# Kernel optimization log

Measured on AMD Instinct MI355X. Metric: run time of the kernel, lower is better.

The kernel has to match this reference:

```python
import jax, jax.numpy as jnp
import numpy as np
from jax import lax

K_TOP = 4
NF1, NF2 = 6, 14
KS1, KS2 = 7, 5


def conv1d_grouped(x, w, b, groups, pad):
    # x: (B, Cin, L), w: (Cout, Cin//groups, K)
    y = lax.conv_general_dilated(x, w, window_strides=(1,), padding=[(pad, pad)],
                                 dimension_numbers=('NCH', 'OIH', 'NCH'),
                                 feature_group_count=groups)
    return y + b[None, :, None]


def kmax_pool(x, k):
    # order-preserving k-max along last axis
    idx = jnp.sort(lax.top_k(x, k)[1], axis=-1)
    return jnp.take_along_axis(x, idx, axis=-1)


def fold_sum(h, b, nf, rows, L):
    # h: (B, rows*nf, L) with group-major channel layout (rows groups of nf)
    h = h.reshape(b, rows, nf, L).transpose(0, 2, 1, 3)        # (B, nf, rows, L)
    h = h.reshape(b, nf, rows // 2, 2, L).sum(axis=3)          # Fold(2,2): sum adjacent row pairs
    return h.transpose(0, 2, 1, 3).reshape(b, (rows // 2) * nf, L)


def setup_inputs() -> dict:
    key = jax.random.key(0)
    ks = jax.random.split(key, 8)
    V, D, C, B, S = 50257, 256, 1000, 32, 1024
    x = jax.random.randint(ks[0], (B, S), 0, V)
    emb = jax.random.normal(ks[1], (V, D), jnp.float32)
    w1 = jax.random.normal(ks[2], (NF1 * D, 1, KS1), jnp.float32) * 0.1
    b1 = jnp.zeros((NF1 * D,), jnp.float32)
    w2 = jax.random.normal(ks[3], (NF2 * (D // 2), NF1, KS2), jnp.float32) * 0.05
    b2 = jnp.zeros((NF2 * (D // 2),), jnp.float32)
    wf = jax.random.normal(ks[4], (C, NF2 * (D // 4) * K_TOP), jnp.float32) * 0.02
    bf = jnp.zeros((C,), jnp.float32)
    return {"x": x, "emb": emb, "w1": w1, "b1": b1, "w2": w2, "b2": b2, "wf": wf, "bf": bf}


def reference(x, emb, w1, b1, w2, b2, wf, bf):
    D = emb.shape[1]
    B = x.shape[0]
    h = emb[x].transpose(0, 2, 1)                 # (B, D, S)
    h = conv1d_grouped(h, w1, b1, groups=D, pad=KS1 - 1)   # (B, 6D, S+6)
    L1 = h.shape[-1]
    h = fold_sum(h, B, NF1, D, L1)                # (B, 3D, L1)
    # dynamic k-max: layer 1 of 2 -> k = max(k_top, ceil(L/2))
    k1 = max(K_TOP, -(-L1 // 2))
    h = jnp.tanh(kmax_pool(h, k1))
    h = conv1d_grouped(h, w2, b2, groups=D // 2, pad=KS2 - 1)  # (B, 7D, k1+4)
    L2 = h.shape[-1]
    h = fold_sum(h, B, NF2, D // 2, L2)           # (B, 14*(D/4), L2)
    h = jnp.tanh(kmax_pool(h, K_TOP))             # (B, 14*(D/4), k_top)
    # dropout is identity in eval mode
    h = h.reshape(B, -1)
    return h @ wf.T + bf
```

## Files before the change

### kernel.cpp

```cpp
#include <hip/hip_runtime.h>
#include <hip/hip_bf16.h>


typedef __attribute__((ext_vector_type(8))) short short8;
typedef __attribute__((ext_vector_type(4))) float f32x4;

__device__ __forceinline__ float fast_tanh(float x) {
    float e = __expf(2.f * x);
    return 1.f - 2.f / (e + 1.f);
}

__device__ __forceinline__ unsigned fkey(float f) {
    unsigned u = __float_as_uint(f);
    return (u & 0x80000000u) ? ~u : (u | 0x80000000u);
}

__device__ __forceinline__ float fkey_inv(unsigned k) {
    unsigned u = (k & 0x80000000u) ? (k ^ 0x80000000u) : ~k;
    return __uint_as_float(u);
}

__device__ __forceinline__ unsigned short f2bf_rne(float f) {
    unsigned u = __float_as_uint(f);
    return (unsigned short)((u + 0x7fffu + ((u >> 16) & 1u)) >> 16);
}

__global__ __launch_bounds__(256) void gather_kernel(
    const int* __restrict__ x, const float* __restrict__ emb, float* __restrict__ E2)
{
    const int b = blockIdx.x >> 4;
    const int c64 = blockIdx.x & 15;
    const int wv = threadIdx.x >> 6, lane = threadIdx.x & 63;
    float* dst = E2 + ((((size_t)b << 6) + lane) << 12);
#pragma unroll
    for (int t = 0; t < 16; ++t) {
        int l = (c64 << 6) + (wv << 4) + t;
        int tok = x[(b << 10) + l];
        float4 v = *(const float4*)(emb + ((size_t)tok << 8) + (lane << 2));
        *(float4*)(dst + (size_t)l * 4) = v;
    }
}

__global__ __launch_bounds__(896) void stage12_kernel(
    const int* __restrict__ x, const float* __restrict__ emb,
    const float* __restrict__ w1, const float* __restrict__ b1,
    const float* __restrict__ w2, const float* __restrict__ b2,
    const float* __restrict__ E2,
    __hip_bfloat16* __restrict__ H)
{
    __shared__ __align__(16) float X[8512];
    __shared__ __align__(16) float F[12 * 536];
    const int b = blockIdx.x >> 6;
    const int r2 = blockIdx.x & 63;
    const int tid = threadIdx.x;
    float* e = X;

    for (int i = tid; i < 12 * 536; i += 896) F[i] = 0.f;
    if (E2) {
        const float* E2blk = E2 + ((((size_t)b << 6) + r2) << 12);
        for (int idx = tid; idx < 1104; idx += 896) {
            int l = idx - 6;
            float4 v = {0.f, 0.f, 0.f, 0.f};
            if (l >= 0 && l < 1024) v = *(const float4*)(E2blk + (size_t)l * 4);
            e[0 * 1104 + idx] = v.x; e[1 * 1104 + idx] = v.y;
            e[2 * 1104 + idx] = v.z; e[3 * 1104 + idx] = v.w;
        }
    } else {
        for (int idx = tid; idx < 1104; idx += 896) {
            int l = idx - 6;
            float4 v = {0.f, 0.f, 0.f, 0.f};
            if (l >= 0 && l < 1024) {
                int tok = x[(b << 10) + l];
                v = *(const float4*)(emb + ((size_t)tok << 8) + (r2 << 2));
            }
            e[0 * 1104 + idx] = v.x; e[1 * 1104 + idx] = v.y;
            e[2 * 1104 + idx] = v.z; e[3 * 1104 + idx] = v.w;
        }
    }
    __syncthreads();

    const int w = tid >> 6;
    const int lane = tid & 63;

    if (w < 12) {
        const int half = (w >= 6) ? 1 : 0;
        const int f = w - half * 6;
        const float* ep0 = e + (2 * half) * 1104;
        const float* ep1 = ep0 + 1104;
        const int c0 = __builtin_amdgcn_readfirstlane((2 * (2 * r2 + half)) * 6 + f);
        const int c1 = c0 + 6;
        float wA[7], wB[7];
#pragma unroll
        for (int t = 0; t < 7; ++t) { wA[t] = w1[c0 * 7 + t]; wB[t] = w1[c1 * 7 + t]; }
        const float bias = b1[c0] + b1[c1];

        const int pos0 = lane * 17;
        float a0[7], a1[7];
#pragma unroll
        for (int t = 0; t < 7; ++t) { a0[t] = ep0[pos0 + t]; a1[t] = ep1[pos0 + t]; }

        unsigned key[17];
#pragma unroll
        for (int j = 0; j < 17; ++j) {
            float a = bias;
#pragma unroll
            for (int t = 0; t < 7; ++t) a += a0[t] * wA[t] + a1[t] * wB[t];
            key[j] = (pos0 + j < 1030) ? fkey(a) : 0u;
            if (j < 16) {
#pragma unroll
                for (int t = 0; t < 6; ++t) { a0[t] = a0[t + 1]; a1[t] = a1[t + 1]; }
                a0[6] = ep0[pos0 + j + 7];
                a1[6] = ep1[pos0 + j + 7];
            }
        }

        unsigned T = 0u;
        for (int bit = 31; bit >= 0; --bit) {
            unsigned cand = T | (1u << bit);
            int cnt = 0;
#pragma unroll
            for (int j = 0; j < 17; ++j) cnt += (int)__popcll(__ballot(key[j] >= cand));
            if (cnt >= 515) T = cand;
            if (cnt == 515) break;
        }

        const unsigned long long lm = (1ull << lane) - 1ull;
        int gt_tot = 0, gt_run = 0, eq_run = 0;
#pragma unroll
        for (int j = 0; j < 17; ++j) {
            unsigned long long bg = __ballot(key[j] > T);
            unsigned long long be = __ballot(key[j] == T);
            gt_tot += (int)__popcll(bg);
            gt_run += (int)__popcll(bg & lm);
            eq_run += (int)__popcll(be & lm);
        }
        const int q = 515 - gt_tot;
        float* Frow = F + w * 536;
#pragma unroll
        for (int j = 0; j < 17; ++j) {
            bool isgt = key[j] > T;
            bool iseq = key[j] == T;
            int pos = gt_run + (eq_run < q ? eq_run : q);
            if (isgt || (iseq && eq_run < q)) Frow[4 + pos] = fast_tanh(fkey_inv(key[j]));
            gt_run += isgt ? 1 : 0;
            eq_run += iseq ? 1 : 0;
        }
    }
    __syncthreads();

    const int jA = lane & 15;
    const int q3 = lane >> 4;
    float* OUT = X;
    short8 Ah0, Ah1, Al0, Al1;
    {
        float wt[16];
#pragma unroll
        for (int mm = 0; mm < 16; ++mm) {
            float v = 0.f;
            if (mm < 15 && jA < 14) {
                const int irow = 3 * q3 + mm / 5;
                const int t = mm % 5;
                const int h2 = (irow >= 6) ? 1 : 0;
                v = w2[(((2 * r2 + h2) * 14 + jA) * 6 + (irow - 6 * h2)) * 5 + t];
            }
            wt[mm] = v;
        }
#pragma unroll
        for (int m = 0; m < 8; ++m) {
            unsigned short h0 = f2bf_rne(wt[m]);
            float fh0 = __uint_as_float((unsigned)h0 << 16);
            Ah0[m] = (short)h0;
            Al0[m] = (short)f2bf_rne(wt[m] - fh0);
            unsigned short h1 = f2bf_rne(wt[8 + m]);
            float fh1 = __uint_as_float((unsigned)h1 << 16);
            Ah1[m] = (short)h1;
            Al1[m] = (short)f2bf_rne(wt[8 + m] - fh1);
        }
    }
    for (int tile = w; tile < 33; tile += 14) {
        const int p0 = tile << 4;
        const int bidx = (3 * q3) * 536 + p0 + jA;
        float fv[16];
#pragma unroll
        for (int mm = 0; mm < 15; ++mm) fv[mm] = F[bidx + (mm / 5) * 536 + (mm % 5)];
        fv[15] = 0.f;
        short8 Bh0, Bh1, Bl0, Bl1;
#pragma unroll
        for (int m = 0; m < 8; ++m) {
            unsigned short h0 = f2bf_rne(fv[m]);
            float fh0 = __uint_as_float((unsigned)h0 << 16);
            Bh0[m] = (short)h0;
            Bl0[m] = (short)f2bf_rne(fv[m] - fh0);
            unsigned short h1 = f2bf_rne(fv[8 + m]);
            float fh1 = __uint_as_float((unsigned)h1 << 16);
            Bh1[m] = (short)h1;
            Bl1[m] = (short)f2bf_rne(fv[8 + m] - fh1);
        }
        f32x4 d0 = {0.f, 0.f, 0.f, 0.f};
        d0 = __builtin_amdgcn_mfma_f32_16x16x32_bf16(Ah0, Bh0, d0, 0, 0, 0);
        d0 = __builtin_amdgcn_mfma_f32_16x16x32_bf16(Ah1, Bh1, d0, 0, 0, 0);
        d0 = __builtin_amdgcn_mfma_f32_16x16x32_bf16(Ah0, Bl0, d0, 0, 0, 0);
        d0 = __builtin_amdgcn_mfma_f32_16x16x32_bf16(Ah1, Bl1, d0, 0, 0, 0);
        d0 = __builtin_amdgcn_mfma_f32_16x16x32_bf16(Al0, Bh0, d0, 0, 0, 0);
        d0 = __builtin_amdgcn_mfma_f32_16x16x32_bf16(Al1, Bh1, d0, 0, 0, 0);
        float* orow = OUT + (q3 * 4) * 532 + p0 + jA;
#pragma unroll
        for (int r = 0; r < 4; ++r) orow[r * 532] = d0[r];
    }
    __syncthreads();

    {
        const int j = w;
        const int base = lane * 9;
        const int bidx2 = __builtin_amdgcn_readfirstlane((2 * r2) * 14 + j);
        const float bias2 = b2[bidx2] + b2[bidx2 + 14];
        float vv[9];
#pragma unroll
        for (int jj = 0; jj < 9; ++jj)
            vv[jj] = (base + jj < 519) ? OUT[j * 532 + base + jj] : -INFINITY;
        float sv[4]; int si[4];
#pragma unroll
        for (int it = 0; it < 4; ++it) {
            float m = vv[0]; int mi = base;
#pragma unroll
            for (int jj = 1; jj < 9; ++jj) { if (vv[jj] > m) { m = vv[jj]; mi = base + jj; } }
#pragma unroll
            for (int d = 1; d < 64; d <<= 1) {
                float om = __shfl_xor(m, d, 64);
                int omi = __shfl_xor(mi, d, 64);
                if (om > m || (om == m && omi < mi)) { m = om; mi = omi; }
            }
            sv[it] = m; si[it] = mi;
            int lj = mi - base;
#pragma unroll
            for (int jj = 0; jj < 9; ++jj) if (jj == lj) vv[jj] = -INFINITY;
        }
#define CSWAP(a, bq) { if (si[a] > si[bq]) { int ti = si[a]; si[a] = si[bq]; si[bq] = ti; \
                                             float tv = sv[a]; sv[a] = sv[bq]; sv[bq] = tv; } }
        CSWAP(0, 1) CSWAP(2, 3) CSWAP(0, 2) CSWAP(1, 3) CSWAP(1, 2)
#undef CSWAP
        if (lane == 0) {
            __hip_bfloat16* op = H + (size_t)b * 3584 + (r2 * 14 + j) * 4;
#pragma unroll
            for (int k = 0; k < 4; ++k) op[k] = __float2bfloat16(fast_tanh(sv[k] + bias2));
        }
    }
}

__global__ __launch_bounds__(256) void bias_init_kernel(
    const float* __restrict__ bfv, float* __restrict__ out)
{
    int idx = blockIdx.x * 256 + threadIdx.x;
    if (idx < 32000) out[idx] = bfv[idx - (idx / 1000) * 1000];
}

__global__ __launch_bounds__(256) void stage3_kernel(
    const __hip_bfloat16* __restrict__ Hb, const float* __restrict__ wf,
    float* __restrict__ out)
{
    __shared__ __align__(16) float sred[2 * 4 * 256];
    const int nt = blockIdx.x % 63;
    const int kc = blockIdx.x / 63;
    const int w = threadIdx.x >> 6, lane = threadIdx.x & 63;
    const int row = lane & 15, quad = lane >> 4;
    const int c = nt * 16 + row;
    const bool cvalid = (c < 1000);
    const int kofs = kc * 896 + w * 224 + quad * 8;
    const __hip_bfloat16* ap0 = Hb + (size_t)row * 3584 + kofs;
    const __hip_bfloat16* ap1 = ap0 + (size_t)16 * 3584;
    const float* bp = wf + (size_t)(cvalid ? c : 0) * 3584 + kofs;

    f32x4 acc0 = {0.f, 0.f, 0.f, 0.f};
    f32x4 acc1 = {0.f, 0.f, 0.f, 0.f};
#pragma unroll
    for (int it = 0; it < 7; ++it) {
        short8 a0 = *(const short8*)(ap0 + it * 32);
        short8 a1 = *(const short8*)(ap1 + it * 32);
        float4 p0 = *(const float4*)(bp + it * 32);
        float4 p1 = *(const float4*)(bp + it * 32 + 4);
        short8 bfr;
        bfr[0] = (short)f2bf_rne(p0.x); bfr[1] = (short)f2bf_rne(p0.y);
        bfr[2] = (short)f2bf_rne(p0.z); bfr[3] = (short)f2bf_rne(p0.w);
        bfr[4] = (short)f2bf_rne(p1.x); bfr[5] = (short)f2bf_rne(p1.y);
        bfr[6] = (short)f2bf_rne(p1.z); bfr[7] = (short)f2bf_rne(p1.w);
        if (!cvalid) bfr = short8{0, 0, 0, 0, 0, 0, 0, 0};
        acc0 = __builtin_amdgcn_mfma_f32_16x16x32_bf16(a0, bfr, acc0, 0, 0, 0);
        acc1 = __builtin_amdgcn_mfma_f32_16x16x32_bf16(a1, bfr, acc1, 0, 0, 0);
    }
#pragma unroll
    for (int r_ = 0; r_ < 4; ++r_) {
        sred[(0 * 4 + w) * 256 + lane * 4 + r_] = acc0[r_];
        sred[(1 * 4 + w) * 256 + lane * 4 + r_] = acc1[r_];
    }
    __syncthreads();
    if (threadIdx.x < 128) {
        const int mt = threadIdx.x >> 6;
        const int l2 = threadIdx.x & 63;
        const int rr = l2 & 15, qq = l2 >> 4;
        const int cc = nt * 16 + rr;
        if (cc < 1000) {
            const float* sp = sred + mt * 4 * 256;
#pragma unroll
            for (int r_ = 0; r_ < 4; ++r_) {
                float s = sp[0 * 256 + l2 * 4 + r_] + sp[1 * 256 + l2 * 4 + r_]
                        + sp[2 * 256 + l2 * 4 + r_] + sp[3 * 256 + l2 * 4 + r_];
                int brow = mt * 16 + qq * 4 + r_;
                atomicAdd(&out[brow * 1000 + cc], s);
            }
        }
    }
}

extern "C" void kernel_launch(void* const* d_in, const int* in_sizes, int n_in,
                              void* d_out, int out_size, void* d_ws, size_t ws_size,
                              hipStream_t stream) {
    const int* x      = (const int*)d_in[0];
    const float* emb  = (const float*)d_in[1];
    const float* w1   = (const float*)d_in[2];
    const float* b1   = (const float*)d_in[3];
    const float* w2   = (const float*)d_in[4];
    const float* b2   = (const float*)d_in[5];
    const float* wf   = (const float*)d_in[6];
    const float* bfv  = (const float*)d_in[7];

    const size_t E2_BYTES = (size_t)32 * 64 * 1024 * 4 * 4;
    const size_t H_BYTES  = (size_t)32 * 3584 * 2;
    float* E2 = nullptr;
    __hip_bfloat16* H;
    if (ws_size >= E2_BYTES + H_BYTES) {
        E2 = (float*)d_ws;
        H = (__hip_bfloat16*)((char*)d_ws + E2_BYTES);
    } else {
        H = (__hip_bfloat16*)d_ws;
    }

    bias_init_kernel<<<125, 256, 0, stream>>>(bfv, (float*)d_out);
    if (E2) gather_kernel<<<32 * 16, 256, 0, stream>>>(x, emb, E2);
    stage12_kernel<<<32 * 64, 896, 0, stream>>>(x, emb, w1, b1, w2, b2, E2, H);
    stage3_kernel<<<63 * 4, 256, 0, stream>>>(H, wf, (float*)d_out);
}
```

Baseline: 273.3 us.

## Drop gather pre-pass, gather embeddings directly in stage12, fuse bias into GEMM

Measured after the change: 270.9 us. No clear change (-0.9%).

```diff
diff --git a/kernel.cpp b/kernel.cpp
--- a/kernel.cpp
+++ b/kernel.cpp
@@ -23,29 +23,12 @@
 __device__ __forceinline__ unsigned short f2bf_rne(float f) {
     unsigned u = __float_as_uint(f);
     return (unsigned short)((u + 0x7fffu + ((u >> 16) & 1u)) >> 16);
-}
-
-__global__ __launch_bounds__(256) void gather_kernel(
-    const int* __restrict__ x, const float* __restrict__ emb, float* __restrict__ E2)
-{
-    const int b = blockIdx.x >> 4;
-    const int c64 = blockIdx.x & 15;
-    const int wv = threadIdx.x >> 6, lane = threadIdx.x & 63;
-    float* dst = E2 + ((((size_t)b << 6) + lane) << 12);
-#pragma unroll
-    for (int t = 0; t < 16; ++t) {
-        int l = (c64 << 6) + (wv << 4) + t;
-        int tok = x[(b << 10) + l];
-        float4 v = *(const float4*)(emb + ((size_t)tok << 8) + (lane << 2));
-        *(float4*)(dst + (size_t)l * 4) = v;
-    }
 }
 
 __global__ __launch_bounds__(896) void stage12_kernel(
     const int* __restrict__ x, const float* __restrict__ emb,
     const float* __restrict__ w1, const float* __restrict__ b1,
     const float* __restrict__ w2, const float* __restrict__ b2,
-    const float* __restrict__ E2,
     __hip_bfloat16* __restrict__ H)
 {
     __shared__ __align__(16) float X[8512];
@@ -55,26 +38,25 @@
     const int tid = threadIdx.x;
     float* e = X;
 
-    for (int i = tid; i < 12 * 536; i += 896) F[i] = 0.f;
-    if (E2) {
-        const float* E2blk = E2 + ((((size_t)b << 6) + r2) << 12);
-        for (int idx = tid; idx < 1104; idx += 896) {
-            int l = idx - 6;
-            float4 v = {0.f, 0.f, 0.f, 0.f};
-            if (l >= 0 && l < 1024) v = *(const float4*)(E2blk + (size_t)l * 4);
-            e[0 * 1104 + idx] = v.x; e[1 * 1104 + idx] = v.y;
-            e[2 * 1104 + idx] = v.z; e[3 * 1104 + idx] = v.w;
-        }
-    } else {
-        for (int idx = tid; idx < 1104; idx += 896) {
-            int l = idx - 6;
-            float4 v = {0.f, 0.f, 0.f, 0.f};
-            if (l >= 0 && l < 1024) {
-                int tok = x[(b << 10) + l];
-                v = *(const float4*)(emb + ((size_t)tok << 8) + (r2 << 2));
-            }
-            e[0 * 1104 + idx] = v.x; e[1 * 1104 + idx] = v.y;
-            e[2 * 1104 + idx] = v.z; e[3 * 1104 + idx] = v.w;
+    {
+        const int l0 = tid - 6;
+        const int l1 = tid + 890;
+        float4 v0 = {0.f, 0.f, 0.f, 0.f}, v1 = {0.f, 0.f, 0.f, 0.f};
+        if (l0 >= 0 && l0 < 1024) {
+            int t0 = x[(b << 10) + l0];
+            v0 = *(const float4*)(emb + ((size_t)t0 << 8) + (r2 << 2));
+        }
+        if (tid < 208 && l1 < 1024) {
+            int t1 = x[(b << 10) + l1];
+            v1 = *(const float4*)(emb + ((size_t)t1 << 8) + (r2 << 2));
+        }
+        for (int i = tid; i < 12 * 536; i += 896) F[i] = 0.f;
+        e[0 * 1104 + tid] = v0.x; e[1 * 1104 + tid] = v0.y;
+        e[2 * 1104 + tid] = v0.z; e[3 * 1104 + tid] = v0.w;
+        if (tid < 208) {
+            const int idx = tid + 896;
+            e[0 * 1104 + idx] = v1.x; e[1 * 1104 + idx] = v1.y;
+            e[2 * 1104 + idx] = v1.z; e[3 * 1104 + idx] = v1.w;
         }
     }
     __syncthreads();
@@ -247,35 +229,25 @@
     }
 }
 
-__global__ __launch_bounds__(256) void bias_init_kernel(
+__global__ __launch_bounds__(256) void stage3_kernel(
+    const __hip_bfloat16* __restrict__ Hb, const float* __restrict__ wf,
     const float* __restrict__ bfv, float* __restrict__ out)
 {
-    int idx = blockIdx.x * 256 + threadIdx.x;
-    if (idx < 32000) out[idx] = bfv[idx - (idx / 1000) * 1000];
-}
-
-__global__ __launch_bounds__(256) void stage3_kernel(
-    const __hip_bfloat16* __restrict__ Hb, const float* __restrict__ wf,
-    float* __restrict__ out)
-{
-    __shared__ __align__(16) float sred[2 * 4 * 256];
+    __shared__ __align__(16) float sred[4 * 256];
     const int nt = blockIdx.x % 63;
-    const int kc = blockIdx.x / 63;
+    const int mh = blockIdx.x / 63;
     const int w = threadIdx.x >> 6, lane = threadIdx.x & 63;
     const int row = lane & 15, quad = lane >> 4;
     const int c = nt * 16 + row;
     const bool cvalid = (c < 1000);
-    const int kofs = kc * 896 + w * 224 + quad * 8;
-    const __hip_bfloat16* ap0 = Hb + (size_t)row * 3584 + kofs;
-    const __hip_bfloat16* ap1 = ap0 + (size_t)16 * 3584;
+    const int kofs = w * 896 + quad * 8;
+    const __hip_bfloat16* ap = Hb + (size_t)(mh * 16 + row) * 3584 + kofs;
     const float* bp = wf + (size_t)(cvalid ? c : 0) * 3584 + kofs;
 
-    f32x4 acc0 = {0.f, 0.f, 0.f, 0.f};
-    f32x4 acc1 = {0.f, 0.f, 0.f, 0.f};
-#pragma unroll
-    for (int it = 0; it < 7; ++it) {
-        short8 a0 = *(const short8*)(ap0 + it * 32);
-        short8 a1 = *(const short8*)(ap1 + it * 32);
+    f32x4 acc = {0.f, 0.f, 0.f, 0.f};
+#pragma unroll
+    for (int it = 0; it < 28; ++it) {
+        short8 a0 = *(const short8*)(ap + it * 32);
         float4 p0 = *(const float4*)(bp + it * 32);
         float4 p1 = *(const float4*)(bp + it * 32 + 4);
         short8 bfr;
@@ -284,28 +256,23 @@
         bfr[4] = (short)f2bf_rne(p1.x); bfr[5] = (short)f2bf_rne(p1.y);
         bfr[6] = (short)f2bf_rne(p1.z); bfr[7] = (short)f2bf_rne(p1.w);
         if (!cvalid) bfr = short8{0, 0, 0, 0, 0, 0, 0, 0};
-        acc0 = __builtin_amdgcn_mfma_f32_16x16x32_bf16(a0, bfr, acc0, 0, 0, 0);
-        acc1 = __builtin_amdgcn_mfma_f32_16x16x32_bf16(a1, bfr, acc1, 0, 0, 0);
-    }
-#pragma unroll
-    for (int r_ = 0; r_ < 4; ++r_) {
-        sred[(0 * 4 + w) * 256 + lane * 4 + r_] = acc0[r_];
-        sred[(1 * 4 + w) * 256 + lane * 4 + r_] = acc1[r_];
-    }
-    __syncthreads();
-    if (threadIdx.x < 128) {
-        const int mt = threadIdx.x >> 6;
-        const int l2 = threadIdx.x & 63;
+        acc = __builtin_amdgcn_mfma_f32_16x16x32_bf16(a0, bfr, acc, 0, 0, 0);
+    }
+#pragma unroll
+    for (int r_ = 0; r_ < 4; ++r_) sred[w * 256 + lane * 4 + r_] = acc[r_];
+    __syncthreads();
+    if (threadIdx.x < 64) {
+        const int l2 = threadIdx.x;
         const int rr = l2 & 15, qq = l2 >> 4;
         const int cc = nt * 16 + rr;
         if (cc < 1000) {
-            const float* sp = sred + mt * 4 * 256;
+            const float bias = bfv[cc];
 #pragma unroll
             for (int r_ = 0; r_ < 4; ++r_) {
-                float s = sp[0 * 256 + l2 * 4 + r_] + sp[1 * 256 + l2 * 4 + r_]
-                        + sp[2 * 256 + l2 * 4 + r_] + sp[3 * 256 + l2 * 4 + r_];
-                int brow = mt * 16 + qq * 4 + r_;
-                atomicAdd(&out[brow * 1000 + cc], s);
+                float s = sred[0 * 256 + l2 * 4 + r_] + sred[1 * 256 + l2 * 4 + r_]
+                        + sred[2 * 256 + l2 * 4 + r_] + sred[3 * 256 + l2 * 4 + r_];
+                int brow = mh * 16 + qq * 4 + r_;
+                out[brow * 1000 + cc] = s + bias;
             }
         }
     }
@@ -323,19 +290,8 @@
     const float* wf   = (const float*)d_in[6];
     const float* bfv  = (const float*)d_in[7];
 
-    const size_t E2_BYTES = (size_t)32 * 64 * 1024 * 4 * 4;
-    const size_t H_BYTES  = (size_t)32 * 3584 * 2;
-    float* E2 = nullptr;
-    __hip_bfloat16* H;
-    if (ws_size >= E2_BYTES + H_BYTES) {
-        E2 = (float*)d_ws;
-        H = (__hip_bfloat16*)((char*)d_ws + E2_BYTES);
-    } else {
-        H = (__hip_bfloat16*)d_ws;
-    }
-
-    bias_init_kernel<<<125, 256, 0, stream>>>(bfv, (float*)d_out);
-    if (E2) gather_kernel<<<32 * 16, 256, 0, stream>>>(x, emb, E2);
-    stage12_kernel<<<32 * 64, 896, 0, stream>>>(x, emb, w1, b1, w2, b2, E2, H);
-    stage3_kernel<<<63 * 4, 256, 0, stream>>>(H, wf, (float*)d_out);
-}
+    __hip_bfloat16* H = (__hip_bfloat16*)d_ws;
+
+    stage12_kernel<<<32 * 64, 896, 0, stream>>>(x, emb, w1, b1, w2, b2, H);
+    stage3_kernel<<<126, 256, 0, stream>>>(H, wf, bfv, (float*)d_out);
+}
```
